# Kernel tuning notes

Measured on AMD Instinct MI355X. Metric: run time of the kernel, lower is better.

## Reference

```python
import jax, jax.numpy as jnp
import numpy as np

B, N, C = 8, 4096, 512
H, DH = 8, 64            # n_heads, d_head -> inner = 512
TED = 1280               # time_embed_dim
M = 64                   # EA per-head dim
INTER = M * H            # 512
MIN_SA = 16


def setup_inputs():
    key = jax.random.key(0)
    ks = jax.random.split(key, 12)
    g = lambda k, shp, s=0.02: (jax.random.normal(k, shp, jnp.float32) * s)
    return dict(
        x=jax.random.normal(ks[0], (B, N, C), jnp.float32),
        t_embedding=jax.random.normal(ks[1], (B, TED), jnp.float32),
        g_w1=g(ks[2], (TED, 64)), g_b1=jnp.zeros((64,), jnp.float32),
        g_w2=g(ks[3], (64, C)), g_b2=jnp.zeros((C,), jnp.float32),
        wq=g(ks[4], (C, H * DH)), wk=g(ks[5], (C, H * DH)), wv=g(ks[6], (C, H * DH)),
        wo=g(ks[7], (H * DH, C)), bo=jnp.zeros((C,), jnp.float32),
        ln_g=jnp.ones((C,), jnp.float32), ln_b=jnp.zeros((C,), jnp.float32),
        ea_k=g(ks[8], (INTER, C), 0.001),  # conv2d weight [inter, C, 1, 1] -> [inter, C]
        ea_v=g(ks[9], (C, INTER), 0.001),  # conv2d weight [C, inter, 1, 1] -> [C, inter]
        alpha=jnp.float32(0.5),
    )


def reference(x, t_embedding, g_w1, g_b1, g_w2, g_b2, wq, wk, wv, wo, bo,
              ln_g, ln_b, ea_k, ea_v, alpha):
    Bx, Nx, Cx = x.shape
    # ---- gating: per-sample channel scores -> per-token importance ----
    hidden = jax.nn.silu(t_embedding @ g_w1 + g_b1)
    local_scores = hidden @ g_w2 + g_b2                      # [B, C]
    imp = jnp.einsum('bqd,bd->bq', x, local_scores)          # [B, N]
    k = max(MIN_SA, int(Nx * 0.1))
    _, idx = jax.lax.top_k(imp, k)                           # [B, k] int32
    x_imp = jnp.take_along_axis(x, idx[:, :, None], axis=1)  # [B, k, C]
    # ---- full self-attention on routed tokens ----
    q = (x_imp @ wq).reshape(Bx, k, H, DH)
    kk = (x_imp @ wk).reshape(Bx, k, H, DH)
    v = (x_imp @ wv).reshape(Bx, k, H, DH)
    sim = jnp.einsum('bihd,bjhd->bhij', q, kk) * (DH ** -0.5)
    attn = jax.nn.softmax(sim, axis=-1)
    sa = jnp.einsum('bhij,bjhd->bihd', attn, v).reshape(Bx, k, H * DH)
    sa = sa @ wo + bo                                        # [B, k, C]
    sa_full = jnp.zeros_like(x).at[jnp.arange(Bx)[:, None], idx].set(sa)
    # ---- external attention branch on all tokens ----
    mu = x.mean(-1, keepdims=True)
    var = x.var(-1, keepdims=True)
    xn = (x - mu) / jnp.sqrt(var + 1e-5) * ln_g + ln_b       # LayerNorm [B, N, C]
    e = jnp.einsum('bnc,ic->bni', xn, ea_k)                  # 1x1 conv -> [B, N, INTER]
    e = e.reshape(Bx, Nx, H, INTER // H)
    a = jax.nn.softmax(e * (M ** -0.5), axis=1)              # softmax over tokens N
    a = a / (a.sum(axis=3, keepdims=True) + 1e-6)            # normalize over head dim
    ea = jnp.einsum('bni,ci->bnc', a.reshape(Bx, Nx, INTER), ea_v)  # [B, N, C]
    return ea + alpha * sa_full
```

## Files before the change

kernel.cpp:

```cpp
#include <hip/hip_runtime.h>
#include <hip/hip_bf16.h>
#include <math.h>

#define B_   8
#define N_   4096
#define C_   512
#define H_   8
#define DH_  64
#define TED_ 1280
#define KSEL 409
#define KPAD 448

typedef __attribute__((ext_vector_type(8))) short bf16x8;
typedef __attribute__((ext_vector_type(4))) float f32x4;

__device__ __forceinline__ unsigned short f2bf(float f) {
  unsigned u = __float_as_uint(f);
  unsigned r = u + 0x7fffu + ((u >> 16) & 1u);
  return (unsigned short)(r >> 16);
}
__device__ __forceinline__ float bf2f(unsigned short s) {
  return __uint_as_float(((unsigned)s) << 16);
}

__device__ __forceinline__ void gload16(const void* g, void* l) {
  __builtin_amdgcn_global_load_lds(
      (const __attribute__((address_space(1))) void*)g,
      (__attribute__((address_space(3))) void*)l,
      16, 0, 0);
}

__global__ __launch_bounds__(256) void k_gating(const float* __restrict__ temb,
    const float* __restrict__ g_w1, const float* __restrict__ g_b1,
    const float* __restrict__ g_w2, const float* __restrict__ g_b2,
    float* __restrict__ scores)
{
  __shared__ float red[256];
  __shared__ float hid[64];
  int b = blockIdx.x, tid = threadIdx.x;
  int j = tid & 63, part = tid >> 6;
  const float* te = temb + b*TED_;
  float s = 0.f;
  for (int t = part*320; t < part*320 + 320; ++t)
    s += te[t] * g_w1[t*64 + j];
  red[tid] = s;
  __syncthreads();
  if (part == 0) {
    float v = red[j] + red[j+64] + red[j+128] + red[j+192] + g_b1[j];
    hid[j] = v / (1.f + __expf(-v));
  }
  __syncthreads();
  for (int c = tid; c < C_; c += 256) {
    float s2 = g_b2[c];
    #pragma unroll 8
    for (int h = 0; h < 64; ++h) s2 += hid[h] * g_w2[h*C_ + c];
    scores[b*C_ + c] = s2;
  }
}

__global__ __launch_bounds__(256) void k_imp_prep(const float* __restrict__ x,
    const float* __restrict__ scores, const float* __restrict__ ln_g,
    const float* __restrict__ ln_b, float* __restrict__ imp,
    unsigned short* __restrict__ xn)
{
  int tid = threadIdx.x, lane = tid & 63, wid = tid >> 6;
  int token = blockIdx.x*4 + wid;
  int b = token >> 12;
  size_t base = (size_t)token*C_ + lane*8;
  float4 v0 = *(const float4*)&x[base];
  float4 v1 = *(const float4*)&x[base + 4];
  const float* sc = scores + b*C_ + lane*8;
  float4 sv0 = *(const float4*)&sc[0];
  float4 sv1 = *(const float4*)&sc[4];
  float si = v0.x*sv0.x + v0.y*sv0.y + v0.z*sv0.z + v0.w*sv0.w
           + v1.x*sv1.x + v1.y*sv1.y + v1.z*sv1.z + v1.w*sv1.w;
  float s1 = v0.x+v0.y+v0.z+v0.w + v1.x+v1.y+v1.z+v1.w;
  float s2 = v0.x*v0.x+v0.y*v0.y+v0.z*v0.z+v0.w*v0.w
           + v1.x*v1.x+v1.y*v1.y+v1.z*v1.z+v1.w*v1.w;
  #pragma unroll
  for (int off = 32; off >= 1; off >>= 1) {
    si += __shfl_xor(si, off, 64);
    s1 += __shfl_xor(s1, off, 64);
    s2 += __shfl_xor(s2, off, 64);
  }
  if (lane == 0) imp[token] = si;
  float m = s1 * (1.f/C_);
  float rs = rsqrtf(s2 * (1.f/C_) - m*m + 1e-5f);
  float4 g0 = *(const float4*)&ln_g[lane*8];
  float4 g1 = *(const float4*)&ln_g[lane*8 + 4];
  float4 b0 = *(const float4*)&ln_b[lane*8];
  float4 b1 = *(const float4*)&ln_b[lane*8 + 4];
  uint4 o;
  o.x = (unsigned)f2bf((v0.x-m)*rs*g0.x + b0.x) | ((unsigned)f2bf((v0.y-m)*rs*g0.y + b0.y) << 16);
  o.y = (unsigned)f2bf((v0.z-m)*rs*g0.z + b0.z) | ((unsigned)f2bf((v0.w-m)*rs*g0.w + b0.w) << 16);
  o.z = (unsigned)f2bf((v1.x-m)*rs*g1.x + b1.x) | ((unsigned)f2bf((v1.y-m)*rs*g1.y + b1.y) << 16);
  o.w = (unsigned)f2bf((v1.z-m)*rs*g1.z + b1.z) | ((unsigned)f2bf((v1.w-m)*rs*g1.w + b1.w) << 16);
  *(uint4*)&xn[base] = o;
}

__global__ __launch_bounds__(256) void k_topk(const float* __restrict__ imp,
                                              int* __restrict__ idxout)
{
  __shared__ unsigned skey[4096];
  __shared__ int hist[256];
  __shared__ unsigned s_prefix;
  __shared__ int s_kneed;
  __shared__ int sc_sel[256], sc_tie[256];
  int b = blockIdx.x, tid = threadIdx.x;
  int lane = tid & 63, wid = tid >> 6;
  for (int i = tid; i < 4096; i += 256) {
    unsigned u = __float_as_uint(imp[b*N_ + i]);
    skey[i] = (u & 0x80000000u) ? ~u : (u | 0x80000000u);
  }
  if (tid == 0) { s_prefix = 0; s_kneed = KSEL; }
  __syncthreads();
  for (int shift = 24; shift >= 0; shift -= 8) {
    hist[tid] = 0;
    __syncthreads();
    unsigned pref = s_prefix;
    int need0 = s_kneed;
    for (int i = tid; i < 4096; i += 256) {
      unsigned key = skey[i];
      bool match = (shift == 24) || ((key >> (shift + 8)) == pref);
      if (match) atomicAdd(&hist[(key >> shift) & 255], 1);
    }
    __syncthreads();
    if (wid == 0) {
      int h0 = hist[lane*4+0], h1 = hist[lane*4+1];
      int h2 = hist[lane*4+2], h3 = hist[lane*4+3];
      int lt = h0 + h1 + h2 + h3;
      int sfx = lt;
      #pragma unroll
      for (int off = 1; off < 64; off <<= 1) {
        int v = __shfl_down(sfx, off, 64);
        sfx += (lane + off < 64) ? v : 0;
      }
      int e3 = sfx - lt;
      int e2 = e3 + h3;
      int e1 = e2 + h2;
      int e0 = e1 + h1;
      int ej0[4] = {e0, e1, e2, e3};
      int hj0[4] = {h0, h1, h2, h3};
      #pragma unroll
      for (int j = 0; j < 4; ++j) {
        if (ej0[j] < need0 && need0 <= ej0[j] + hj0[j]) {
          s_prefix = (pref << 8) | (unsigned)(lane*4 + j);
          s_kneed = need0 - ej0[j];
        }
      }
    }
    __syncthreads();
  }
  unsigned T = s_prefix;
  int tie_take = s_kneed;
  int lc_sel = 0, lc_tie = 0;
  int i0 = tid * 16;
  for (int e2 = 0; e2 < 16; ++e2) {
    unsigned key = skey[i0 + e2];
    lc_sel += (key > T);
    lc_tie += (key == T);
  }
  sc_sel[tid] = lc_sel; sc_tie[tid] = lc_tie;
  __syncthreads();
  for (int off = 1; off < 256; off <<= 1) {
    int a = 0, c2 = 0;
    if (tid >= off) { a = sc_sel[tid - off]; c2 = sc_tie[tid - off]; }
    __syncthreads();
    sc_sel[tid] += a; sc_tie[tid] += c2;
    __syncthreads();
  }
  int total_gt = sc_sel[255];
  int ps = sc_sel[tid] - lc_sel, pt = sc_tie[tid] - lc_tie;
  for (int e2 = 0; e2 < 16; ++e2) {
    int i = i0 + e2;
    unsigned key = skey[i];
    if (key > T) { idxout[b*KSEL + ps] = i; ++ps; }
    else if (key == T) { if (pt < tie_take) idxout[b*KSEL + total_gt + pt] = i; ++pt; }
  }
}

__global__ __launch_bounds__(256) void k_cvt2(const float* __restrict__ sa,
    const float* __restrict__ sb, unsigned short* __restrict__ da,
    unsigned short* __restrict__ db)
{
  const float* src = blockIdx.y ? sb : sa;
  unsigned short* dst = blockIdx.y ? db : da;
  int i = (blockIdx.x*256 + threadIdx.x)*4;
  float4 v = *(const float4*)&src[i];
  unsigned lo = (unsigned)f2bf(v.x) | ((unsigned)f2bf(v.y) << 16);
  unsigned hi = (unsigned)f2bf(v.z) | ((unsigned)f2bf(v.w) << 16);
  uint2 o; o.x = lo; o.y = hi;
  *(uint2*)&dst[i] = o;
}

__global__ __launch_bounds__(256) void k_cvt_t4(
    const float* __restrict__ w0, const float* __restrict__ w1,
    const float* __restrict__ w2, const float* __restrict__ w3,
    unsigned short* __restrict__ t0, unsigned short* __restrict__ t1,
    unsigned short* __restrict__ t2, unsigned short* __restrict__ t3)
{
  int wsel = blockIdx.y;
  const float* W = (wsel == 0) ? w0 : (wsel == 1) ? w1 : (wsel == 2) ? w2 : w3;
  unsigned short* Wt = (wsel == 0) ? t0 : (wsel == 1) ? t1 : (wsel == 2) ? t2 : t3;
  int idx = blockIdx.x*256 + threadIdx.x;
  int o = idx & 511;
  int ig = (idx >> 9) * 8;
  unsigned short r[8];
  #pragma unroll
  for (int j = 0; j < 8; ++j) r[j] = f2bf(W[(size_t)(ig + j)*512 + o]);
  uint4 v;
  v.x = (unsigned)r[0] | ((unsigned)r[1] << 16);
  v.y = (unsigned)r[2] | ((unsigned)r[3] << 16);
  v.z = (unsigned)r[4] | ((unsigned)r[5] << 16);
  v.w = (unsigned)r[6] | ((unsigned)r[7] << 16);
  *(uint4*)&Wt[(size_t)o*512 + ig] = v;
}

__global__ __launch_bounds__(256) void k_gather(const float* __restrict__ x,
    const int* __restrict__ idx, unsigned short* __restrict__ xg)
{
  int tid = threadIdx.x, lane = tid & 63, wid = tid >> 6;
  int gr = blockIdx.x*4 + wid;
  int b = gr / KPAD, r = gr - b*KPAD;
  uint4 o;
  if (r < KSEL) {
    int tok = idx[b*KSEL + r];
    size_t base = ((size_t)b*N_ + tok)*C_ + lane*8;
    float4 v0 = *(const float4*)&x[base];
    float4 v1 = *(const float4*)&x[base + 4];
    o.x = (unsigned)f2bf(v0.x) | ((unsigned)f2bf(v0.y) << 16);
    o.y = (unsigned)f2bf(v0.z) | ((unsigned)f2bf(v0.w) << 16);
    o.z = (unsigned)f2bf(v1.x) | ((unsigned)f2bf(v1.y) << 16);
    o.w = (unsigned)f2bf(v1.z) | ((unsigned)f2bf(v1.w) << 16);
  } else {
    o.x = o.y = o.z = o.w = 0u;
  }
  *(uint4*)&xg[(size_t)gr*C_ + lane*8] = o;
}

__device__ __forceinline__ void stage128(const unsigned short* __restrict__ Arows,
    const unsigned short* __restrict__ Brows, int k0,
    unsigned short* As, unsigned short* Bs, int srow, int spos)
{
  #pragma unroll
  for (int s = 0; s < 4; ++s) {
    int row = s*32 + srow;
    int chunk = spos ^ (row & 7);
    gload16(&Arows[(size_t)row*C_ + k0 + chunk*8], &As[row*64 + spos*8]);
    gload16(&Brows[(size_t)row*C_ + k0 + chunk*8], &Bs[row*64 + spos*8]);
  }
}

__device__ __forceinline__ void gemm128_pipe(
    const unsigned short* __restrict__ Arows,
    const unsigned short* __restrict__ Brows,
    unsigned short* As, unsigned short* Bs,
    f32x4 acc[4][4])
{
  int tid = threadIdx.x;
  int lane = tid & 63, wid = tid >> 6;
  int wr = wid >> 1, wc = wid & 1;
  int srow = tid >> 3, spos = tid & 7;
  int l15 = lane & 15, lh = lane >> 4;
  stage128(Arows, Brows, 0, As, Bs, srow, spos);
  __syncthreads();
  for (int t = 0; t < 8; ++t) {
    int cur = (t & 1) ? 8192 : 0;
    int nxt = 8192 - cur;
    if (t < 7)
      stage128(Arows, Brows, (t+1)*64, As + nxt, Bs + nxt, srow, spos);
    #pragma unroll
    for (int kk = 0; kk < 2; ++kk) {
      bf16x8 af[4], bfr[4];
      #pragma unroll
      for (int m = 0; m < 4; ++m) {
        int row = wr*64 + m*16 + l15;
        int chunk = (kk*4 + lh) ^ (row & 7);
        af[m] = *(const bf16x8*)&As[cur + row*64 + chunk*8];
      }
      #pragma unroll
      for (int n = 0; n < 4; ++n) {
        int row = wc*64 + n*16 + l15;
        int chunk = (kk*4 + lh) ^ (row & 7);
        bfr[n] = *(const bf16x8*)&Bs[cur + row*64 + chunk*8];
      }
      #pragma unroll
      for (int m = 0; m < 4; ++m)
        #pragma unroll
        for (int n = 0; n < 4; ++n)
          acc[m][n] = __builtin_amdgcn_mfma_f32_16x16x32_bf16(af[m], bfr[n], acc[m][n], 0, 0, 0);
    }
    __syncthreads();
  }
}

__global__ __launch_bounds__(256) void k_eak_gemm(
    const unsigned short* __restrict__ A,
    const unsigned short* __restrict__ Bm,
    unsigned short* __restrict__ e, float* __restrict__ colsum)
{
  __shared__ unsigned short As[2*8192];
  __shared__ unsigned short Bs[2*8192];
  __shared__ float csum[128];
  int tid = threadIdx.x;
  int m0 = blockIdx.x * 128, n0 = blockIdx.y * 128;
  int lane = tid & 63, wid = tid >> 6;
  int wr = wid >> 1, wc = wid & 1;
  int l15 = lane & 15, lh = lane >> 4;
  f32x4 acc[4][4];
  #pragma unroll
  for (int m = 0; m < 4; ++m)
    #pragma unroll
    for (int n = 0; n < 4; ++n) acc[m][n] = (f32x4){0.f,0.f,0.f,0.f};
  gemm128_pipe(A + (size_t)m0*C_, Bm + (size_t)n0*C_, As, Bs, acc);
  unsigned short* tile = As;
  if (tid < 128) csum[tid] = 0.f;
  __syncthreads();
  float pc[4] = {0.f, 0.f, 0.f, 0.f};
  #pragma unroll
  for (int m = 0; m < 4; ++m) {
    int row = wr*64 + m*16 + lh*4;
    #pragma unroll
    for (int n = 0; n < 4; ++n) {
      int col = wc*64 + n*16 + l15;
      #pragma unroll
      for (int r = 0; r < 4; ++r) {
        float v = acc[m][n][r] * 0.125f;
        tile[(row + r)*128 + col] = f2bf(v);
        pc[n] += __expf(v);
      }
    }
  }
  #pragma unroll
  for (int n = 0; n < 4; ++n)
    atomicAdd(&csum[wc*64 + n*16 + l15], pc[n]);
  __syncthreads();
  int bb = blockIdx.x >> 5;
  #pragma unroll
  for (int j = 0; j < 8; ++j) {
    int lin = j*256 + tid;
    int row = lin >> 4, seg = lin & 15;
    *(uint4*)&e[(size_t)(m0 + row)*C_ + n0 + seg*8] = *(const uint4*)&tile[row*128 + seg*8];
  }
  if (tid < 128) atomicAdd(&colsum[bb*C_ + n0 + tid], csum[tid]);
}

__global__ __launch_bounds__(256) void k_eav_gemm(
    const unsigned short* __restrict__ A,
    const unsigned short* __restrict__ Bm,
    float* __restrict__ Co)
{
  __shared__ unsigned short As[2*8192];
  __shared__ unsigned short Bs[2*8192];
  int tid = threadIdx.x;
  int m0 = blockIdx.x * 128, n0 = blockIdx.y * 128;
  int lane = tid & 63, wid = tid >> 6;
  int wr = wid >> 1, wc = wid & 1;
  int l15 = lane & 15, lh = lane >> 4;
  f32x4 acc[4][4];
  #pragma unroll
  for (int m = 0; m < 4; ++m)
    #pragma unroll
    for (int n = 0; n < 4; ++n) acc[m][n] = (f32x4){0.f,0.f,0.f,0.f};
  gemm128_pipe(A + (size_t)m0*C_, Bm + (size_t)n0*C_, As, Bs, acc);
  #pragma unroll
  for (int m = 0; m < 4; ++m) {
    int row = m0 + wr*64 + m*16 + lh*4;
    #pragma unroll
    for (int n = 0; n < 4; ++n) {
      int col = n0 + wc*64 + n*16 + l15;
      #pragma unroll
      for (int r = 0; r < 4; ++r)
        Co[(size_t)(row + r)*C_ + col] = acc[m][n][r];
    }
  }
}

__global__ __launch_bounds__(256) void k_qkv_gemm(
    const unsigned short* __restrict__ xg,
    const unsigned short* __restrict__ wqt,
    const unsigned short* __restrict__ wkt,
    const unsigned short* __restrict__ wvt,
    unsigned short* __restrict__ qg, unsigned short* __restrict__ kg,
    unsigned short* __restrict__ vt)
{
  __shared__ unsigned short As[2*8192];
  __shared__ unsigned short Bs[2*8192];
  int tid = threadIdx.x;
  int m0 = blockIdx.x * 128, n0 = blockIdx.y * 128, w = blockIdx.z;
  const unsigned short* Wt = (w == 0) ? wqt : (w == 1) ? wkt : wvt;
  int lane = tid & 63, wid = tid >> 6;
  int wr = wid >> 1, wc = wid & 1;
  int l15 = lane & 15, lh = lane >> 4;
  f32x4 acc[4][4];
  #pragma unroll
  for (int m = 0; m < 4; ++m)
    #pragma unroll
    for (int n = 0; n < 4; ++n) acc[m][n] = (f32x4){0.f,0.f,0.f,0.f};
  gemm128_pipe(xg + (size_t)m0*C_, Wt + (size_t)n0*C_, As, Bs, acc);
  float scale = (w == 0) ? 0.125f : 1.f;
  #pragma unroll
  for (int m = 0; m < 4; ++m) {
    int rowl = wr*64 + m*16 + lh*4;
    #pragma unroll
    for (int n = 0; n < 4; ++n) {
      int col = n0 + wc*64 + n*16 + l15;
      int h = col >> 6, d = col & 63;
      #pragma unroll
      for (int r = 0; r < 4; ++r) {
        int mr = m0 + rowl + r;
        int b = mr / KPAD, rr = mr - b*KPAD;
        unsigned short v = f2bf(acc[m][n][r] * scale);
        if (w < 2) {
          unsigned short* dst = (w == 0) ? qg : kg;
          dst[(((size_t)(b*H_ + h))*KPAD + rr)*DH_ + d] = v;
        } else {
          vt[(((size_t)(b*H_ + h))*DH_ + d)*KPAD + rr] = v;
        }
      }
    }
  }
}

__global__ __launch_bounds__(256) void k_attn_mfma(
    const unsigned short* __restrict__ qg, const unsigned short* __restrict__ kg,
    const unsigned short* __restrict__ vt, unsigned short* __restrict__ sab)
{
  __shared__ unsigned short Qs[4096], Ps[4096];
  __shared__ unsigned short Ks[2][4096], Vs[2][4096];
  int tid = threadIdx.x, lane = tid & 63, wid = tid >> 6;
  int qt = blockIdx.x, h = blockIdx.y, b = blockIdx.z;
  int l15 = lane & 15, lh = lane >> 4;
  const unsigned short* qbase = qg + (((size_t)(b*H_ + h))*KPAD + qt*64)*DH_;
  const unsigned short* kbase = kg + ((size_t)(b*H_ + h))*KPAD*DH_;
  const unsigned short* vbase = vt + ((size_t)(b*H_ + h))*DH_*KPAD;
  int c0 = tid, c1 = tid + 256;
  int r0 = c0 >> 3, p0 = c0 & 7;
  int r1 = c1 >> 3, p1 = c1 & 7;
  gload16(&qbase[(size_t)r0*64 + (p0 ^ (r0 & 7))*8], &Qs[c0*8]);
  gload16(&qbase[(size_t)r1*64 + (p1 ^ (r1 & 7))*8], &Qs[c1*8]);
  gload16(&kbase[(size_t)r0*64 + (p0 ^ (r0 & 7))*8], &Ks[0][c0*8]);
  gload16(&kbase[(size_t)r1*64 + (p1 ^ (r1 & 7))*8], &Ks[0][c1*8]);
  gload16(&vbase[(size_t)r0*KPAD + (p0 ^ (r0 & 7))*8], &Vs[0][c0*8]);
  gload16(&vbase[(size_t)r1*KPAD + (p1 ^ (r1 & 7))*8], &Vs[0][c1*8]);
  __syncthreads();

  f32x4 acc_o[4];
  #pragma unroll
  for (int ct = 0; ct < 4; ++ct) acc_o[ct] = (f32x4){0.f,0.f,0.f,0.f};
  float m_run[4], l_run[4];
  #pragma unroll
  for (int r = 0; r < 4; ++r) { m_run[r] = -1e30f; l_run[r] = 0.f; }

  for (int t = 0; t < 7; ++t) {
    int cur = t & 1;
    if (t < 6) {
      int kt1 = (t+1)*64;
      int nb = cur ^ 1;
      gload16(&kbase[((size_t)(kt1 + r0))*64 + (p0 ^ (r0 & 7))*8], &Ks[nb][c0*8]);
      gload16(&kbase[((size_t)(kt1 + r1))*64 + (p1 ^ (r1 & 7))*8], &Ks[nb][c1*8]);
      gload16(&vbase[(size_t)r0*KPAD + kt1 + (p0 ^ (r0 & 7))*8], &Vs[nb][c0*8]);
      gload16(&vbase[(size_t)r1*KPAD + kt1 + (p1 ^ (r1 & 7))*8], &Vs[nb][c1*8]);
    }
    int kt0 = t*64;

    f32x4 s4[4];
    #pragma unroll
    for (int ct = 0; ct < 4; ++ct) s4[ct] = (f32x4){0.f,0.f,0.f,0.f};
    #pragma unroll
    for (int ks = 0; ks < 2; ++ks) {
      int qrow = wid*16 + l15;
      int qch = (ks*4 + lh) ^ (qrow & 7);
      bf16x8 qa = *(const bf16x8*)&Qs[qrow*64 + qch*8];
      #pragma unroll
      for (int ct = 0; ct < 4; ++ct) {
        int krow = ct*16 + l15;
        int kch = (ks*4 + lh) ^ (krow & 7);
        bf16x8 kb8 = *(const bf16x8*)&Ks[cur][krow*64 + kch*8];
        s4[ct] = __builtin_amdgcn_mfma_f32_16x16x32_bf16(qa, kb8, s4[ct], 0, 0, 0);
      }
    }

    bool valid[4];
    #pragma unroll
    for (int ct = 0; ct < 4; ++ct) valid[ct] = (kt0 + ct*16 + l15) < KSEL;
    #pragma unroll
    for (int r = 0; r < 4; ++r) {
      float sv[4];
      #pragma unroll
      for (int ct = 0; ct < 4; ++ct) sv[ct] = valid[ct] ? s4[ct][r] : -1e30f;
      float tm = fmaxf(fmaxf(sv[0], sv[1]), fmaxf(sv[2], sv[3]));
      #pragma unroll
      for (int off = 1; off < 16; off <<= 1) tm = fmaxf(tm, __shfl_xor(tm, off, 64));
      float mnew = fmaxf(m_run[r], tm);
      float corr = __expf(m_run[r] - mnew);
      float rs = 0.f;
      float p[4];
      #pragma unroll
      for (int ct = 0; ct < 4; ++ct) { p[ct] = __expf(sv[ct] - mnew); rs += p[ct]; }
      #pragma unroll
      for (int off = 1; off < 16; off <<= 1) rs += __shfl_xor(rs, off, 64);
      l_run[r] = l_run[r]*corr + rs;
      m_run[r] = mnew;
      #pragma unroll
      for (int ct = 0; ct < 4; ++ct) acc_o[ct][r] *= corr;
      int rowL = wid*16 + lh*4 + r;
      #pragma unroll
      for (int ct = 0; ct < 4; ++ct) {
        int col = ct*16 + l15;
        Ps[rowL*64 + ((col >> 3) ^ (rowL & 7))*8 + (col & 7)] = f2bf(p[ct]);
      }
    }

    #pragma unroll
    for (int ks = 0; ks < 2; ++ks) {
      int prow = wid*16 + l15;
      int pch = (ks*4 + lh) ^ (prow & 7);
      bf16x8 pa = *(const bf16x8*)&Ps[prow*64 + pch*8];
      #pragma unroll
      for (int ct = 0; ct < 4; ++ct) {
        int vrow = ct*16 + l15;
        int vch = (ks*4 + lh) ^ (vrow & 7);
        bf16x8 vb8 = *(const bf16x8*)&Vs[cur][vrow*64 + vch*8];
        acc_o[ct] = __builtin_amdgcn_mfma_f32_16x16x32_bf16(pa, vb8, acc_o[ct], 0, 0, 0);
      }
    }
    __syncthreads();
  }

  #pragma unroll
  for (int r = 0; r < 4; ++r) {
    int rg = qt*64 + wid*16 + lh*4 + r;
    float inv = 1.f / l_run[r];
    #pragma unroll
    for (int ct = 0; ct < 4; ++ct) {
      int col = h*64 + ct*16 + l15;
      unsigned short v = (rg < KSEL) ? f2bf(acc_o[ct][r] * inv) : (unsigned short)0;
      sab[((size_t)b*KPAD + rg)*C_ + col] = v;
    }
  }
}

__global__ __launch_bounds__(256) void k_saout_gemm(
    const unsigned short* __restrict__ sab,
    const unsigned short* __restrict__ wot,
    const float* __restrict__ bo, const int* __restrict__ idx,
    const float* __restrict__ alphap, float* __restrict__ out)
{
  __shared__ unsigned short As[2*8192];
  __shared__ unsigned short Bs[2*8192];
  int tid = threadIdx.x;
  int m0 = blockIdx.x * 128, n0 = blockIdx.y * 128;
  int lane = tid & 63, wid = tid >> 6;
  int wr = wid >> 1, wc = wid & 1;
  int l15 = lane & 15, lh = lane >> 4;
  f32x4 acc[4][4];
  #pragma unroll
  for (int m = 0; m < 4; ++m)
    #pragma unroll
    for (int n = 0; n < 4; ++n) acc[m][n] = (f32x4){0.f,0.f,0.f,0.f};
  gemm128_pipe(sab + (size_t)m0*C_, wot + (size_t)n0*C_, As, Bs, acc);
  float alpha = alphap[0];
  #pragma unroll
  for (int m = 0; m < 4; ++m) {
    int rowl = wr*64 + m*16 + lh*4;
    #pragma unroll
    for (int r = 0; r < 4; ++r) {
      int mr = m0 + rowl + r;
      int b = mr / KPAD, rr = mr - b*KPAD;
      if (rr < KSEL) {
        int token = idx[b*KSEL + rr];
        size_t obase = ((size_t)b*N_ + token)*C_;
        #pragma unroll
        for (int n = 0; n < 4; ++n) {
          int col = n0 + wc*64 + n*16 + l15;
          out[obase + col] += alpha*(acc[m][n][r] + bo[col]);
        }
      }
    }
  }
}

__global__ __launch_bounds__(256) void k_anorm(const unsigned short* __restrict__ e,
    const float* __restrict__ colsum, unsigned short* __restrict__ ab)
{
  int tid = threadIdx.x, lane = tid & 63, wid = tid >> 6;
  int token = blockIdx.x*4 + wid;
  int b = token >> 12;
  size_t base = (size_t)token*C_ + lane*8;
  uint4 w = *(const uint4*)&e[base];
  float f[8];
  f[0] = __uint_as_float(w.x << 16); f[1] = __uint_as_float(w.x & 0xffff0000u);
  f[2] = __uint_as_float(w.y << 16); f[3] = __uint_as_float(w.y & 0xffff0000u);
  f[4] = __uint_as_float(w.z << 16); f[5] = __uint_as_float(w.z & 0xffff0000u);
  f[6] = __uint_as_float(w.w << 16); f[7] = __uint_as_float(w.w & 0xffff0000u);
  const float* cs = colsum + b*C_ + lane*8;
  float4 c0 = *(const float4*)&cs[0];
  float4 c1 = *(const float4*)&cs[4];
  float a[8];
  a[0] = __expf(f[0])/c0.x; a[1] = __expf(f[1])/c0.y;
  a[2] = __expf(f[2])/c0.z; a[3] = __expf(f[3])/c0.w;
  a[4] = __expf(f[4])/c1.x; a[5] = __expf(f[5])/c1.y;
  a[6] = __expf(f[6])/c1.z; a[7] = __expf(f[7])/c1.w;
  float hs = a[0]+a[1]+a[2]+a[3]+a[4]+a[5]+a[6]+a[7];
  hs += __shfl_xor(hs, 1, 64);
  hs += __shfl_xor(hs, 2, 64);
  hs += __shfl_xor(hs, 4, 64);
  hs += 1e-6f;
  float r = 1.f / hs;
  uint4 o;
  o.x = (unsigned)f2bf(a[0]*r) | ((unsigned)f2bf(a[1]*r) << 16);
  o.y = (unsigned)f2bf(a[2]*r) | ((unsigned)f2bf(a[3]*r) << 16);
  o.z = (unsigned)f2bf(a[4]*r) | ((unsigned)f2bf(a[5]*r) << 16);
  o.w = (unsigned)f2bf(a[6]*r) | ((unsigned)f2bf(a[7]*r) << 16);
  *(uint4*)&ab[base] = o;
}

extern "C" void kernel_launch(void* const* d_in, const int* in_sizes, int n_in,
                              void* d_out, int out_size, void* d_ws, size_t ws_size,
                              hipStream_t stream)
{
  const float* x     = (const float*)d_in[0];
  const float* temb  = (const float*)d_in[1];
  const float* g_w1  = (const float*)d_in[2];
  const float* g_b1  = (const float*)d_in[3];
  const float* g_w2  = (const float*)d_in[4];
  const float* g_b2  = (const float*)d_in[5];
  const float* wq    = (const float*)d_in[6];
  const float* wk    = (const float*)d_in[7];
  const float* wv    = (const float*)d_in[8];
  const float* wo    = (const float*)d_in[9];
  const float* bo    = (const float*)d_in[10];
  const float* ln_g  = (const float*)d_in[11];
  const float* ln_b  = (const float*)d_in[12];
  const float* ea_k  = (const float*)d_in[13];
  const float* ea_v  = (const float*)d_in[14];
  const float* alpha = (const float*)d_in[15];
  float* out = (float*)d_out;
  float* ws = (float*)d_ws;

  float* scores  = ws;
  float* colsum  = ws;
  float* imp     = ws + 4096;
  int*   idx     = (int*)(ws + 102400);
  unsigned short* ebuf = (unsigned short*)(ws + 106496);
  unsigned short* xnb  = (unsigned short*)(ws + 8495104);
  unsigned short* eakb = (unsigned short*)(ws + 16883712);
  unsigned short* eavb = (unsigned short*)(ws + 17014784);
  unsigned short* wqt  = (unsigned short*)(ws + 17145856);
  unsigned short* wkt  = (unsigned short*)(ws + 17276928);
  unsigned short* wvt  = (unsigned short*)(ws + 17408000);
  unsigned short* wot  = (unsigned short*)(ws + 17539072);
  unsigned short* xg   = (unsigned short*)(ws + 17670144);
  unsigned short* qg   = (unsigned short*)(ws + 18587648);
  unsigned short* kg   = (unsigned short*)(ws + 19505152);
  unsigned short* vtb  = (unsigned short*)(ws + 20422656);
  unsigned short* sab  = (unsigned short*)(ws + 21340160);

  k_gating     <<<dim3(B_),          dim3(256), 0, stream>>>(temb, g_w1, g_b1, g_w2, g_b2, scores);
  k_imp_prep   <<<dim3(B_*N_/4),     dim3(256), 0, stream>>>(x, scores, ln_g, ln_b, imp, xnb);
  k_topk       <<<dim3(B_),          dim3(256), 0, stream>>>(imp, idx);
  hipMemsetAsync(colsum, 0, 4096*sizeof(float), stream);
  k_cvt2       <<<dim3(256, 2),      dim3(256), 0, stream>>>(ea_k, ea_v, eakb, eavb);
  k_cvt_t4     <<<dim3(128, 4),      dim3(256), 0, stream>>>(wq, wk, wv, wo, wqt, wkt, wvt, wot);
  k_gather     <<<dim3(B_*KPAD/4),   dim3(256), 0, stream>>>(x, idx, xg);
  k_qkv_gemm   <<<dim3(28, 4, 3),    dim3(256), 0, stream>>>(xg, wqt, wkt, wvt, qg, kg, vtb);
  k_attn_mfma  <<<dim3(7, H_, B_),   dim3(256), 0, stream>>>(qg, kg, vtb, sab);
  k_eak_gemm   <<<dim3(256, 4),      dim3(256), 0, stream>>>(xnb, eakb, ebuf, colsum);
  k_anorm      <<<dim3(B_*N_/4),     dim3(256), 0, stream>>>(ebuf, colsum, xnb);
  k_eav_gemm   <<<dim3(256, 4),      dim3(256), 0, stream>>>(xnb, eavb, out);
  k_saout_gemm <<<dim3(28, 4),       dim3(256), 0, stream>>>(sab, wot, bo, idx, alpha, out);
}
```

Measured before the change: 198.0 us.

## Fuse sparse attention output into EA-V GEMM epilogue via inverse index map

```diff
diff --git a/kernel.cpp b/kernel.cpp
--- a/kernel.cpp
+++ b/kernel.cpp
@@ -99,7 +99,8 @@
 }
 
 __global__ __launch_bounds__(256) void k_topk(const float* __restrict__ imp,
-                                              int* __restrict__ idxout)
+                                              int* __restrict__ idxout,
+                                              int* __restrict__ inv)
 {
   __shared__ unsigned skey[4096];
   __shared__ int hist[256];
@@ -174,8 +175,13 @@
   for (int e2 = 0; e2 < 16; ++e2) {
     int i = i0 + e2;
     unsigned key = skey[i];
-    if (key > T) { idxout[b*KSEL + ps] = i; ++ps; }
-    else if (key == T) { if (pt < tie_take) idxout[b*KSEL + total_gt + pt] = i; ++pt; }
+    int v = -1;
+    if (key > T) { idxout[b*KSEL + ps] = i; v = ps; ++ps; }
+    else if (key == T) {
+      if (pt < tie_take) { idxout[b*KSEL + total_gt + pt] = i; v = total_gt + pt; }
+      ++pt;
+    }
+    inv[b*N_ + i] = v;
   }
 }
 
@@ -238,6 +244,50 @@
   *(uint4*)&xg[(size_t)gr*C_ + lane*8] = o;
 }
 
+__device__ __forceinline__ void gemm128_body(
+    const unsigned short* __restrict__ Arows,
+    const unsigned short* __restrict__ Brows,
+    unsigned short* As, unsigned short* Bs, f32x4 acc[4][4])
+{
+  int tid = threadIdx.x;
+  int lane = tid & 63, wid = tid >> 6;
+  int wr = wid >> 1, wc = wid & 1;
+  int srow = tid >> 3, spos = tid & 7;
+  int l15 = lane & 15, lh = lane >> 4;
+  for (int k0 = 0; k0 < C_; k0 += 64) {
+    #pragma unroll
+    for (int s = 0; s < 4; ++s) {
+      int row = s*32 + srow;
+      int chunk = spos ^ (row & 7);
+      gload16(&Arows[(size_t)row*C_ + k0 + chunk*8], &As[row*64 + spos*8]);
+      gload16(&Brows[(size_t)row*C_ + k0 + chunk*8], &Bs[row*64 + spos*8]);
+    }
+    __syncthreads();
+    #pragma unroll
+    for (int kk = 0; kk < 2; ++kk) {
+      bf16x8 af[4], bfr[4];
+      #pragma unroll
+      for (int m = 0; m < 4; ++m) {
+        int row = wr*64 + m*16 + l15;
+        int chunk = (kk*4 + lh) ^ (row & 7);
+        af[m] = *(const bf16x8*)&As[row*64 + chunk*8];
+      }
+      #pragma unroll
+      for (int n = 0; n < 4; ++n) {
+        int row = wc*64 + n*16 + l15;
+        int chunk = (kk*4 + lh) ^ (row & 7);
+        bfr[n] = *(const bf16x8*)&Bs[row*64 + chunk*8];
+      }
+      #pragma unroll
+      for (int m = 0; m < 4; ++m)
+        #pragma unroll
+        for (int n = 0; n < 4; ++n)
+          acc[m][n] = __builtin_amdgcn_mfma_f32_16x16x32_bf16(af[m], bfr[n], acc[m][n], 0, 0, 0);
+    }
+    __syncthreads();
+  }
+}
+
 __device__ __forceinline__ void stage128(const unsigned short* __restrict__ Arows,
     const unsigned short* __restrict__ Brows, int k0,
     unsigned short* As, unsigned short* Bs, int srow, int spos)
@@ -299,11 +349,13 @@
     const unsigned short* __restrict__ Bm,
     unsigned short* __restrict__ e, float* __restrict__ colsum)
 {
-  __shared__ unsigned short As[2*8192];
-  __shared__ unsigned short Bs[2*8192];
+  __shared__ unsigned short As[8192];
+  __shared__ unsigned short Bs[8192];
   __shared__ float csum[128];
   int tid = threadIdx.x;
-  int m0 = blockIdx.x * 128, n0 = blockIdx.y * 128;
+  int bid = blockIdx.x;
+  int swz = (bid & 7)*128 + (bid >> 3);
+  int m0 = (swz >> 2) * 128, n0 = (swz & 3) * 128;
   int lane = tid & 63, wid = tid >> 6;
   int wr = wid >> 1, wc = wid & 1;
   int l15 = lane & 15, lh = lane >> 4;
@@ -312,21 +364,20 @@
   for (int m = 0; m < 4; ++m)
     #pragma unroll
     for (int n = 0; n < 4; ++n) acc[m][n] = (f32x4){0.f,0.f,0.f,0.f};
-  gemm128_pipe(A + (size_t)m0*C_, Bm + (size_t)n0*C_, As, Bs, acc);
-  unsigned short* tile = As;
+  gemm128_body(A + (size_t)m0*C_, Bm + (size_t)n0*C_, As, Bs, acc);
   if (tid < 128) csum[tid] = 0.f;
   __syncthreads();
   float pc[4] = {0.f, 0.f, 0.f, 0.f};
   #pragma unroll
   for (int m = 0; m < 4; ++m) {
-    int row = wr*64 + m*16 + lh*4;
-    #pragma unroll
-    for (int n = 0; n < 4; ++n) {
-      int col = wc*64 + n*16 + l15;
-      #pragma unroll
-      for (int r = 0; r < 4; ++r) {
+    int row = m0 + wr*64 + m*16 + lh*4;
+    #pragma unroll
+    for (int r = 0; r < 4; ++r) {
+      #pragma unroll
+      for (int n = 0; n < 4; ++n) {
+        int col = n0 + wc*64 + n*16 + l15;
         float v = acc[m][n][r] * 0.125f;
-        tile[(row + r)*128 + col] = f2bf(v);
+        e[(size_t)(row + r)*C_ + col] = f2bf(v);
         pc[n] += __expf(v);
       }
     }
@@ -335,25 +386,22 @@
   for (int n = 0; n < 4; ++n)
     atomicAdd(&csum[wc*64 + n*16 + l15], pc[n]);
   __syncthreads();
-  int bb = blockIdx.x >> 5;
-  #pragma unroll
-  for (int j = 0; j < 8; ++j) {
-    int lin = j*256 + tid;
-    int row = lin >> 4, seg = lin & 15;
-    *(uint4*)&e[(size_t)(m0 + row)*C_ + n0 + seg*8] = *(const uint4*)&tile[row*128 + seg*8];
-  }
+  int bb = m0 >> 12;
   if (tid < 128) atomicAdd(&colsum[bb*C_ + n0 + tid], csum[tid]);
 }
 
 __global__ __launch_bounds__(256) void k_eav_gemm(
     const unsigned short* __restrict__ A,
     const unsigned short* __restrict__ Bm,
+    const int* __restrict__ inv, const float* __restrict__ sad,
     float* __restrict__ Co)
 {
-  __shared__ unsigned short As[2*8192];
-  __shared__ unsigned short Bs[2*8192];
+  __shared__ unsigned short As[8192];
+  __shared__ unsigned short Bs[8192];
   int tid = threadIdx.x;
-  int m0 = blockIdx.x * 128, n0 = blockIdx.y * 128;
+  int bid = blockIdx.x;
+  int swz = (bid & 7)*128 + (bid >> 3);
+  int m0 = (swz >> 2) * 128, n0 = (swz & 3) * 128;
   int lane = tid & 63, wid = tid >> 6;
   int wr = wid >> 1, wc = wid & 1;
   int l15 = lane & 15, lh = lane >> 4;
@@ -362,16 +410,23 @@
   for (int m = 0; m < 4; ++m)
     #pragma unroll
     for (int n = 0; n < 4; ++n) acc[m][n] = (f32x4){0.f,0.f,0.f,0.f};
-  gemm128_pipe(A + (size_t)m0*C_, Bm + (size_t)n0*C_, As, Bs, acc);
+  gemm128_body(A + (size_t)m0*C_, Bm + (size_t)n0*C_, As, Bs, acc);
   #pragma unroll
   for (int m = 0; m < 4; ++m) {
-    int row = m0 + wr*64 + m*16 + lh*4;
-    #pragma unroll
-    for (int n = 0; n < 4; ++n) {
-      int col = n0 + wc*64 + n*16 + l15;
-      #pragma unroll
-      for (int r = 0; r < 4; ++r)
-        Co[(size_t)(row + r)*C_ + col] = acc[m][n][r];
+    int rowl = wr*64 + m*16 + lh*4;
+    #pragma unroll
+    for (int r = 0; r < 4; ++r) {
+      int row = m0 + rowl + r;
+      int iv = inv[row];
+      int b = row >> 12;
+      const float* sap = sad + ((size_t)(b*KPAD) + (iv < 0 ? 0 : iv))*C_;
+      #pragma unroll
+      for (int n = 0; n < 4; ++n) {
+        int col = n0 + wc*64 + n*16 + l15;
+        float v = acc[m][n][r];
+        if (iv >= 0) v += sap[col];
+        Co[(size_t)row*C_ + col] = v;
+      }
     }
   }
 }
@@ -544,8 +599,8 @@
 __global__ __launch_bounds__(256) void k_saout_gemm(
     const unsigned short* __restrict__ sab,
     const unsigned short* __restrict__ wot,
-    const float* __restrict__ bo, const int* __restrict__ idx,
-    const float* __restrict__ alphap, float* __restrict__ out)
+    const float* __restrict__ bo,
+    const float* __restrict__ alphap, float* __restrict__ sad)
 {
   __shared__ unsigned short As[2*8192];
   __shared__ unsigned short Bs[2*8192];
@@ -567,15 +622,10 @@
     #pragma unroll
     for (int r = 0; r < 4; ++r) {
       int mr = m0 + rowl + r;
-      int b = mr / KPAD, rr = mr - b*KPAD;
-      if (rr < KSEL) {
-        int token = idx[b*KSEL + rr];
-        size_t obase = ((size_t)b*N_ + token)*C_;
-        #pragma unroll
-        for (int n = 0; n < 4; ++n) {
-          int col = n0 + wc*64 + n*16 + l15;
-          out[obase + col] += alpha*(acc[m][n][r] + bo[col]);
-        }
+      #pragma unroll
+      for (int n = 0; n < 4; ++n) {
+        int col = n0 + wc*64 + n*16 + l15;
+        sad[(size_t)mr*C_ + col] = alpha*(acc[m][n][r] + bo[col]);
       }
     }
   }
@@ -642,6 +692,7 @@
   float* scores  = ws;
   float* colsum  = ws;
   float* imp     = ws + 4096;
+  int*   invm    = (int*)(ws + 4096);
   int*   idx     = (int*)(ws + 102400);
   unsigned short* ebuf = (unsigned short*)(ws + 106496);
   unsigned short* xnb  = (unsigned short*)(ws + 8495104);
@@ -656,18 +707,19 @@
   unsigned short* kg   = (unsigned short*)(ws + 19505152);
   unsigned short* vtb  = (unsigned short*)(ws + 20422656);
   unsigned short* sab  = (unsigned short*)(ws + 21340160);
+  float* sad = ws + 18587648;
 
   k_gating     <<<dim3(B_),          dim3(256), 0, stream>>>(temb, g_w1, g_b1, g_w2, g_b2, scores);
   k_imp_prep   <<<dim3(B_*N_/4),     dim3(256), 0, stream>>>(x, scores, ln_g, ln_b, imp, xnb);
-  k_topk       <<<dim3(B_),          dim3(256), 0, stream>>>(imp, idx);
+  k_topk       <<<dim3(B_),          dim3(256), 0, stream>>>(imp, idx, invm);
   hipMemsetAsync(colsum, 0, 4096*sizeof(float), stream);
   k_cvt2       <<<dim3(256, 2),      dim3(256), 0, stream>>>(ea_k, ea_v, eakb, eavb);
   k_cvt_t4     <<<dim3(128, 4),      dim3(256), 0, stream>>>(wq, wk, wv, wo, wqt, wkt, wvt, wot);
   k_gather     <<<dim3(B_*KPAD/4),   dim3(256), 0, stream>>>(x, idx, xg);
   k_qkv_gemm   <<<dim3(28, 4, 3),    dim3(256), 0, stream>>>(xg, wqt, wkt, wvt, qg, kg, vtb);
   k_attn_mfma  <<<dim3(7, H_, B_),   dim3(256), 0, stream>>>(qg, kg, vtb, sab);
-  k_eak_gemm   <<<dim3(256, 4),      dim3(256), 0, stream>>>(xnb, eakb, ebuf, colsum);
+  k_eak_gemm   <<<dim3(1024),        dim3(256), 0, stream>>>(xnb, eakb, ebuf, colsum);
   k_anorm      <<<dim3(B_*N_/4),     dim3(256), 0, stream>>>(ebuf, colsum, xnb);
-  k_eav_gemm   <<<dim3(256, 4),      dim3(256), 0, stream>>>(xnb, eavb, out);
-  k_saout_gemm <<<dim3(28, 4),       dim3(256), 0, stream>>>(sab, wot, bo, idx, alpha, out);
-}
+  k_saout_gemm <<<dim3(28, 4),       dim3(256), 0, stream>>>(sab, wot, bo, alpha, sad);
+  k_eav_gemm   <<<dim3(1024),        dim3(256), 0, stream>>>(xnb, eavb, invm, sad, out);
+}
```

Measured after the change: 201.2 us. Within noise of the previous version (+1.6%).
